# Kernel optimization log

Hardware: AMD Instinct MI355X
Metric: run time of the kernel (lower is better)

The kernel has to match this reference:

```python
import jax, jax.numpy as jnp
import numpy as np

TEMPERATURE = 0.04
LAMBDA_KOLEO = 0.1
EPS_NORM = 1e-12
EPS_KOLEO = 1e-9


def setup_inputs() -> dict:
    key = jax.random.key(0)
    k1, k2 = jax.random.split(key)
    N, D = 8192, 512
    z1 = jax.random.normal(k1, (N, D), dtype=jnp.float32)
    z2 = jax.random.normal(k2, (N, D), dtype=jnp.float32)
    return {"z1": z1, "z2": z2}


def _l2_normalize(x):
    # matches F.normalize(x, dim=1) with default eps=1e-12
    n = jnp.linalg.norm(x, axis=1, keepdims=True)
    return x / jnp.maximum(n, EPS_NORM)


def _infonce(queries, keys, temperature):
    # [N, N] similarity logits; labels are the diagonal
    logits = (queries @ keys.T) / temperature
    logp = jax.nn.log_softmax(logits, axis=1)
    return -jnp.mean(jnp.diagonal(logp))


def _koleo(emb):
    # pairwise euclidean distances via gram trick (matches torch.cdist p=2)
    sq = jnp.sum(emb * emb, axis=1)
    d2 = sq[:, None] + sq[None, :] - 2.0 * (emb @ emb.T)
    d = jnp.sqrt(jnp.maximum(d2, 0.0))
    N = emb.shape[0]
    eye = jnp.eye(N, dtype=bool)
    d = jnp.where(eye, jnp.inf, d)
    min_d = jnp.min(d, axis=1)
    return -jnp.mean(jnp.log(min_d + EPS_KOLEO))


def reference(z1, z2):
    z1 = _l2_normalize(z1)
    z2 = _l2_normalize(z2)
    loss_12 = _infonce(z1, z2, TEMPERATURE)
    loss_21 = _infonce(z2, z1, TEMPERATURE)
    loss_contrastive = (loss_12 + loss_21) / 2
    koleo_1 = _koleo(z1)
    koleo_2 = _koleo(z2)
    loss_koleo = (koleo_1 + koleo_2) / 2
    total_loss = loss_contrastive + LAMBDA_KOLEO * loss_koleo
    return total_loss
```

## Files before the change

### kernel.cpp

```cpp
#include <hip/hip_runtime.h>
#include <hip/hip_bf16.h>
#include <hip/hip_fp8.h>
#include <math.h>

#define N 8192
#define D 512
#define BM 128
#define BK 64
#define NSTRIP 64
#define S_BLOCKS (NSTRIP * NSTRIP)
#define TRI (NSTRIP * (NSTRIP + 1) / 2)
#define G_BLOCKS (2 * TRI)
#define SG_BLOCKS (S_BLOCKS + G_BLOCKS)

typedef float f32x4 __attribute__((ext_vector_type(4)));
typedef long l2 __attribute__((ext_vector_type(2)));

__device__ inline void gload_lds16(const void* g, void* l) {
  __builtin_amdgcn_global_load_lds(
      (const __attribute__((address_space(1))) void*)g,
      (__attribute__((address_space(3))) void*)l, 16, 0, 0);
}

__global__ __launch_bounds__(256) void norm_kernel(
    const float* __restrict__ z1, const float* __restrict__ z2,
    unsigned char* __restrict__ q1, unsigned char* __restrict__ q2,
    float* __restrict__ diag, float* __restrict__ out) {
  int row = blockIdx.x;
  int t = threadIdx.x;
  if (row == 0 && t == 0) out[0] = 0.0f;
  const float* a = z1 + (size_t)row * D;
  const float* b = z2 + (size_t)row * D;
  float va[2], vb[2];
  float ss1 = 0.f, ss2 = 0.f, dd = 0.f;
#pragma unroll
  for (int i = 0; i < 2; i++) {
    float x = a[t + 256 * i];
    float y = b[t + 256 * i];
    va[i] = x; vb[i] = y;
    ss1 += x * x; ss2 += y * y; dd += x * y;
  }
#pragma unroll
  for (int off = 1; off < 64; off <<= 1) {
    ss1 += __shfl_xor(ss1, off);
    ss2 += __shfl_xor(ss2, off);
    dd  += __shfl_xor(dd,  off);
  }
  __shared__ float red[3][4];
  int wv = t >> 6;
  if ((t & 63) == 0) { red[0][wv] = ss1; red[1][wv] = ss2; red[2][wv] = dd; }
  __syncthreads();
  ss1 = red[0][0] + red[0][1] + red[0][2] + red[0][3];
  ss2 = red[1][0] + red[1][1] + red[1][2] + red[1][3];
  dd  = red[2][0] + red[2][1] + red[2][2] + red[2][3];
  float i1 = 1.0f / fmaxf(sqrtf(ss1), 1e-12f);
  float i2 = 1.0f / fmaxf(sqrtf(ss2), 1e-12f);
#pragma unroll
  for (int i = 0; i < 2; i++) {
    __hip_fp8_e4m3 c1((float)(va[i] * i1));
    __hip_fp8_e4m3 c2((float)(vb[i] * i2));
    q1[(size_t)row * D + t + 256 * i] = c1.__x;
    q2[(size_t)row * D + t + 256 * i] = c2.__x;
  }
  if (t == 0) diag[row] = dd * i1 * i2;
}

__device__ __forceinline__ void mm_tile_fp8(
    const unsigned char* __restrict__ X, const unsigned char* __restrict__ Y,
    int r0, int c0, unsigned char* At, unsigned char* Bt, f32x4 (&acc)[4][4],
    int t, int lr, int quad, int rw, int cw) {
  const f32x4 vzero = {0.0f, 0.0f, 0.0f, 0.0f};
#pragma unroll
  for (int i = 0; i < 4; i++)
#pragma unroll
    for (int j = 0; j < 4; j++) acc[i][j] = vzero;

  for (int kc = 0; kc < 8; kc++) {
    int k0 = kc * BK;
    __syncthreads();
#pragma unroll
    for (int it = 0; it < 2; it++) {
      int s = it * 256 + t;
      int row = s >> 2, cs = s & 3;
      int src = cs ^ ((row >> 1) & 3);
      gload_lds16(X + (size_t)(r0 + row) * D + k0 + src * 16, &At[s * 16]);
    }
#pragma unroll
    for (int it = 0; it < 2; it++) {
      int s = it * 256 + t;
      int row = s >> 2, cs = s & 3;
      int src = cs ^ ((row >> 1) & 3);
      gload_lds16(Y + (size_t)(c0 + row) * D + k0 + src * 16, &Bt[s * 16]);
    }
    __syncthreads();

    l2 af[4], bf[4];
#pragma unroll
    for (int i = 0; i < 4; i++) {
      int row = rw * 64 + i * 16 + lr;
      int ps = quad ^ ((row >> 1) & 3);
      af[i] = *(const l2*)&At[row * 64 + ps * 16];
    }
#pragma unroll
    for (int j = 0; j < 4; j++) {
      int row = cw * 64 + j * 16 + lr;
      int ps = quad ^ ((row >> 1) & 3);
      bf[j] = *(const l2*)&Bt[row * 64 + ps * 16];
    }
#pragma unroll
    for (int i = 0; i < 4; i++)
#pragma unroll
      for (int j = 0; j < 4; j++)
        acc[i][j] = __builtin_amdgcn_mfma_f32_16x16x32_fp8_fp8(af[i].x, bf[j].x, acc[i][j], 0, 0, 0);
#pragma unroll
    for (int i = 0; i < 4; i++)
#pragma unroll
      for (int j = 0; j < 4; j++)
        acc[i][j] = __builtin_amdgcn_mfma_f32_16x16x32_fp8_fp8(af[i].y, bf[j].y, acc[i][j], 0, 0, 0);
  }
}

__global__ __launch_bounds__(256, 3) void sg_kernel(
    const unsigned char* __restrict__ q1, const unsigned char* __restrict__ q2,
    float* __restrict__ rowS, float* __restrict__ colS,
    float* __restrict__ partG) {
  __shared__ unsigned char At[BM * BK];
  __shared__ unsigned char Bt[BM * BK];
  __shared__ float redA[2][BM];
  __shared__ float redB[2][BM];

  int bx = blockIdx.x;
  int t = threadIdx.x;
  int lane = t & 63;
  int wave = t >> 6;
  int quad = lane >> 4;
  int lr = lane & 15;
  int rw = wave >> 1;
  int cw = wave & 1;
  const float scale = 1.4426950408889634f / 0.04f;

  bool smode = bx < S_BLOCKS;
  const unsigned char* X;
  const unsigned char* Y;
  int r0, c0, ga = 0, gb = 0, gg = 0;
  bool diagb = false;
  if (smode) {
    r0 = (bx >> 6) * BM;
    c0 = (bx & 63) * BM;
    X = q1; Y = q2;
  } else {
    int gx = bx - S_BLOCKS;
    gg = (gx >= TRI) ? 1 : 0;
    int tri = gx - gg * TRI;
    int a = (int)((sqrtf(8.0f * (float)tri + 1.0f) - 1.0f) * 0.5f);
    while ((a + 1) * (a + 2) / 2 <= tri) a++;
    while (a * (a + 1) / 2 > tri) a--;
    int b = tri - a * (a + 1) / 2;
    ga = a; gb = b;
    X = gg ? q2 : q1; Y = X;
    r0 = a * BM;
    c0 = b * BM;
    diagb = (a == b);
  }

  f32x4 acc[4][4];
  mm_tile_fp8(X, Y, r0, c0, At, Bt, acc, t, lr, quad, rw, cw);

  if (smode) {
    float rowacc[4][4];
    float colacc[4] = {0.0f, 0.0f, 0.0f, 0.0f};
#pragma unroll
    for (int i = 0; i < 4; i++)
#pragma unroll
      for (int r = 0; r < 4; r++) rowacc[i][r] = 0.0f;
#pragma unroll
    for (int i = 0; i < 4; i++)
#pragma unroll
      for (int j = 0; j < 4; j++)
#pragma unroll
        for (int r = 0; r < 4; r++) {
          float e = __builtin_amdgcn_exp2f(acc[i][j][r] * scale);
          rowacc[i][r] += e;
          colacc[j] += e;
        }
#pragma unroll
    for (int j = 0; j < 4; j++) {
      colacc[j] += __shfl_xor(colacc[j], 16);
      colacc[j] += __shfl_xor(colacc[j], 32);
    }
    if (lane < 16) {
#pragma unroll
      for (int j = 0; j < 4; j++) redA[rw][cw * 64 + j * 16 + lr] = colacc[j];
    }
    __syncthreads();
    if (t < BM) colS[(size_t)(r0 >> 7) * N + c0 + t] = redA[0][t] + redA[1][t];

#pragma unroll
    for (int i = 0; i < 4; i++)
#pragma unroll
      for (int r = 0; r < 4; r++) {
        float v = rowacc[i][r];
#pragma unroll
        for (int off = 1; off < 16; off <<= 1) v += __shfl_xor(v, off);
        if (lr == 0) redB[cw][rw * 64 + i * 16 + quad * 4 + r] = v;
      }
    __syncthreads();
    if (t < BM) rowS[(size_t)(c0 >> 7) * N + r0 + t] = redB[0][t] + redB[1][t];
  } else {
#pragma unroll
    for (int i = 0; i < 4; i++)
#pragma unroll
      for (int r = 0; r < 4; r++) {
        int rr = rw * 64 + i * 16 + quad * 4 + r;
        float v = -3.0e38f;
#pragma unroll
        for (int j = 0; j < 4; j++) {
          float x = acc[i][j][r];
          int cc = cw * 64 + j * 16 + lr;
          if (diagb && cc == rr) x = -3.0e38f;
          v = fmaxf(v, x);
        }
#pragma unroll
        for (int off = 1; off < 16; off <<= 1) v = fmaxf(v, __shfl_xor(v, off));
        if (lr == 0) redA[cw][rr] = v;
      }
    __syncthreads();
    if (t < BM)
      partG[((size_t)(gg * NSTRIP + gb)) * N + r0 + t] = fmaxf(redA[0][t], redA[1][t]);

    if (!diagb) {
#pragma unroll
      for (int j = 0; j < 4; j++) {
        float m = acc[0][j][0];
#pragma unroll
        for (int i = 0; i < 4; i++)
#pragma unroll
          for (int r = 0; r < 4; r++) m = fmaxf(m, acc[i][j][r]);
        m = fmaxf(m, __shfl_xor(m, 16));
        m = fmaxf(m, __shfl_xor(m, 32));
        if (lane < 16) redB[rw][cw * 64 + j * 16 + lr] = m;
      }
      __syncthreads();
      if (t < BM)
        partG[((size_t)(gg * NSTRIP + ga)) * N + c0 + t] = fmaxf(redB[0][t], redB[1][t]);
    }
  }
}

__global__ __launch_bounds__(256) void combine_kernel(
    const float* __restrict__ diag,
    const float* __restrict__ rowS, const float* __restrict__ colS,
    const float* __restrict__ partG, float* __restrict__ out) {
  const float invT = 25.0f;
  int i = blockIdx.x * 256 + threadIdx.x;

  float s = 0.0f;
  for (int q = 0; q < NSTRIP; q++) s += rowS[(size_t)q * N + i];
  float a12 = logf(s) - diag[i] * invT;

  s = 0.0f;
  for (int o = 0; o < NSTRIP; o++) s += colS[(size_t)o * N + i];
  float a21 = logf(s) - diag[i] * invT;

  float g1 = -3.0e38f, g2 = -3.0e38f;
  for (int o = 0; o < NSTRIP; o++) {
    g1 = fmaxf(g1, partG[(size_t)o * N + i]);
    g2 = fmaxf(g2, partG[(size_t)(NSTRIP + o) * N + i]);
  }
  float k1 = logf(sqrtf(fmaxf(2.0f - 2.0f * g1, 0.0f)) + 1e-9f);
  float k2 = logf(sqrtf(fmaxf(2.0f - 2.0f * g2, 0.0f)) + 1e-9f);

  float c = 0.5f * (a12 + a21) / (float)N - 0.1f * 0.5f * (k1 + k2) / (float)N;
#pragma unroll
  for (int off = 1; off < 64; off <<= 1) c += __shfl_xor(c, off);
  __shared__ float fr[4];
  int wv = threadIdx.x >> 6;
  if ((threadIdx.x & 63) == 0) fr[wv] = c;
  __syncthreads();
  if (threadIdx.x == 0)
    atomicAdd(out, fr[0] + fr[1] + fr[2] + fr[3]);
}

extern "C" void kernel_launch(void* const* d_in, const int* in_sizes, int n_in,
                              void* d_out, int out_size, void* d_ws, size_t ws_size,
                              hipStream_t stream) {
  const float* z1 = (const float*)d_in[0];
  const float* z2 = (const float*)d_in[1];
  char* w = (char*)d_ws;
  unsigned char* q1 = (unsigned char*)w; w += (size_t)N * D;
  unsigned char* q2 = (unsigned char*)w; w += (size_t)N * D;
  float* diag = (float*)w;   w += (size_t)N * sizeof(float);
  float* rowS = (float*)w;   w += (size_t)NSTRIP * N * sizeof(float);
  float* colS = (float*)w;   w += (size_t)NSTRIP * N * sizeof(float);
  float* partG = (float*)w;  w += (size_t)2 * NSTRIP * N * sizeof(float);
  float* out = (float*)d_out;

  norm_kernel<<<N, 256, 0, stream>>>(z1, z2, q1, q2, diag, out);
  sg_kernel<<<SG_BLOCKS, 256, 0, stream>>>(q1, q2, rowS, colS, partG);
  combine_kernel<<<N / 256, 256, 0, stream>>>(diag, rowS, colS, partG, out);
}
```

Before: 190.7 us.

## Switch similarity GEMMs from fp8 to int8 MFMA with per-row scales

Quantizes normalized rows to int8 using a per-row absmax scale instead of fp8 e4m3, and runs the GEMMs with the int8 16x16x64 MFMA and a 128-byte K tile. The per-row scales are stored and applied in the epilogue before the exp and max reductions. The aim is to take advantage of int8 MFMA throughput and fewer K iterations, at the cost of extra scale loads and multiplies in the epilogue and doubled LDS tiles, which may lower occupancy.

```diff
diff --git a/kernel.cpp b/kernel.cpp
--- a/kernel.cpp
+++ b/kernel.cpp
@@ -1,20 +1,18 @@
 #include <hip/hip_runtime.h>
 #include <hip/hip_bf16.h>
-#include <hip/hip_fp8.h>
 #include <math.h>
 
 #define N 8192
 #define D 512
 #define BM 128
-#define BK 64
+#define BKB 128
 #define NSTRIP 64
 #define S_BLOCKS (NSTRIP * NSTRIP)
 #define TRI (NSTRIP * (NSTRIP + 1) / 2)
 #define G_BLOCKS (2 * TRI)
 #define SG_BLOCKS (S_BLOCKS + G_BLOCKS)
 
-typedef float f32x4 __attribute__((ext_vector_type(4)));
-typedef long l2 __attribute__((ext_vector_type(2)));
+typedef int i32x4 __attribute__((ext_vector_type(4)));
 
 __device__ inline void gload_lds16(const void* g, void* l) {
   __builtin_amdgcn_global_load_lds(
@@ -25,6 +23,7 @@
 __global__ __launch_bounds__(256) void norm_kernel(
     const float* __restrict__ z1, const float* __restrict__ z2,
     unsigned char* __restrict__ q1, unsigned char* __restrict__ q2,
+    float* __restrict__ invs1, float* __restrict__ invs2,
     float* __restrict__ diag, float* __restrict__ out) {
   int row = blockIdx.x;
   int t = threadIdx.x;
@@ -55,77 +54,97 @@
   dd  = red[2][0] + red[2][1] + red[2][2] + red[2][3];
   float i1 = 1.0f / fmaxf(sqrtf(ss1), 1e-12f);
   float i2 = 1.0f / fmaxf(sqrtf(ss2), 1e-12f);
+  float m1 = 1e-30f, m2 = 1e-30f;
 #pragma unroll
   for (int i = 0; i < 2; i++) {
-    __hip_fp8_e4m3 c1((float)(va[i] * i1));
-    __hip_fp8_e4m3 c2((float)(vb[i] * i2));
-    q1[(size_t)row * D + t + 256 * i] = c1.__x;
-    q2[(size_t)row * D + t + 256 * i] = c2.__x;
-  }
-  if (t == 0) diag[row] = dd * i1 * i2;
-}
-
-__device__ __forceinline__ void mm_tile_fp8(
+    m1 = fmaxf(m1, fabsf(va[i] * i1));
+    m2 = fmaxf(m2, fabsf(vb[i] * i2));
+  }
+#pragma unroll
+  for (int off = 1; off < 64; off <<= 1) {
+    m1 = fmaxf(m1, __shfl_xor(m1, off));
+    m2 = fmaxf(m2, __shfl_xor(m2, off));
+  }
+  __syncthreads();
+  if ((t & 63) == 0) { red[0][wv] = m1; red[1][wv] = m2; }
+  __syncthreads();
+  m1 = fmaxf(fmaxf(red[0][0], red[0][1]), fmaxf(red[0][2], red[0][3]));
+  m2 = fmaxf(fmaxf(red[1][0], red[1][1]), fmaxf(red[1][2], red[1][3]));
+  float s1 = 127.0f / m1, s2 = 127.0f / m2;
+#pragma unroll
+  for (int i = 0; i < 2; i++) {
+    int qa = __float2int_rn(va[i] * i1 * s1);
+    int qb = __float2int_rn(vb[i] * i2 * s2);
+    q1[(size_t)row * D + t + 256 * i] = (unsigned char)qa;
+    q2[(size_t)row * D + t + 256 * i] = (unsigned char)qb;
+  }
+  if (t == 0) {
+    diag[row] = dd * i1 * i2;
+    invs1[row] = m1 * (1.0f / 127.0f);
+    invs2[row] = m2 * (1.0f / 127.0f);
+  }
+}
+
+__device__ __forceinline__ void mm_tile_i8(
     const unsigned char* __restrict__ X, const unsigned char* __restrict__ Y,
-    int r0, int c0, unsigned char* At, unsigned char* Bt, f32x4 (&acc)[4][4],
+    int r0, int c0, unsigned char* At, unsigned char* Bt, i32x4 (&acc)[4][4],
     int t, int lr, int quad, int rw, int cw) {
-  const f32x4 vzero = {0.0f, 0.0f, 0.0f, 0.0f};
+  const i32x4 izero = {0, 0, 0, 0};
 #pragma unroll
   for (int i = 0; i < 4; i++)
 #pragma unroll
-    for (int j = 0; j < 4; j++) acc[i][j] = vzero;
-
-  for (int kc = 0; kc < 8; kc++) {
-    int k0 = kc * BK;
-    __syncthreads();
-#pragma unroll
-    for (int it = 0; it < 2; it++) {
+    for (int j = 0; j < 4; j++) acc[i][j] = izero;
+
+  for (int kc = 0; kc < 4; kc++) {
+    int k0 = kc * BKB;
+    __syncthreads();
+#pragma unroll
+    for (int it = 0; it < 4; it++) {
       int s = it * 256 + t;
-      int row = s >> 2, cs = s & 3;
-      int src = cs ^ ((row >> 1) & 3);
+      int row = s >> 3, cs = s & 7;
+      int src = cs ^ (row & 7);
       gload_lds16(X + (size_t)(r0 + row) * D + k0 + src * 16, &At[s * 16]);
     }
 #pragma unroll
-    for (int it = 0; it < 2; it++) {
+    for (int it = 0; it < 4; it++) {
       int s = it * 256 + t;
-      int row = s >> 2, cs = s & 3;
-      int src = cs ^ ((row >> 1) & 3);
+      int row = s >> 3, cs = s & 7;
+      int src = cs ^ (row & 7);
       gload_lds16(Y + (size_t)(c0 + row) * D + k0 + src * 16, &Bt[s * 16]);
     }
     __syncthreads();
 
-    l2 af[4], bf[4];
-#pragma unroll
-    for (int i = 0; i < 4; i++) {
-      int row = rw * 64 + i * 16 + lr;
-      int ps = quad ^ ((row >> 1) & 3);
-      af[i] = *(const l2*)&At[row * 64 + ps * 16];
-    }
-#pragma unroll
-    for (int j = 0; j < 4; j++) {
-      int row = cw * 64 + j * 16 + lr;
-      int ps = quad ^ ((row >> 1) & 3);
-      bf[j] = *(const l2*)&Bt[row * 64 + ps * 16];
-    }
-#pragma unroll
-    for (int i = 0; i < 4; i++)
-#pragma unroll
-      for (int j = 0; j < 4; j++)
-        acc[i][j] = __builtin_amdgcn_mfma_f32_16x16x32_fp8_fp8(af[i].x, bf[j].x, acc[i][j], 0, 0, 0);
-#pragma unroll
-    for (int i = 0; i < 4; i++)
-#pragma unroll
-      for (int j = 0; j < 4; j++)
-        acc[i][j] = __builtin_amdgcn_mfma_f32_16x16x32_fp8_fp8(af[i].y, bf[j].y, acc[i][j], 0, 0, 0);
+#pragma unroll
+    for (int step = 0; step < 2; step++) {
+      i32x4 af[4], bf[4];
+#pragma unroll
+      for (int i = 0; i < 4; i++) {
+        int row = rw * 64 + i * 16 + lr;
+        int ps = (step * 4 + quad) ^ (row & 7);
+        af[i] = *(const i32x4*)&At[row * BKB + ps * 16];
+      }
+#pragma unroll
+      for (int j = 0; j < 4; j++) {
+        int row = cw * 64 + j * 16 + lr;
+        int ps = (step * 4 + quad) ^ (row & 7);
+        bf[j] = *(const i32x4*)&Bt[row * BKB + ps * 16];
+      }
+#pragma unroll
+      for (int i = 0; i < 4; i++)
+#pragma unroll
+        for (int j = 0; j < 4; j++)
+          acc[i][j] = __builtin_amdgcn_mfma_i32_16x16x64_i8(af[i], bf[j], acc[i][j], 0, 0, 0);
+    }
   }
 }
 
 __global__ __launch_bounds__(256, 3) void sg_kernel(
     const unsigned char* __restrict__ q1, const unsigned char* __restrict__ q2,
+    const float* __restrict__ invs1, const float* __restrict__ invs2,
     float* __restrict__ rowS, float* __restrict__ colS,
     float* __restrict__ partG) {
-  __shared__ unsigned char At[BM * BK];
-  __shared__ unsigned char Bt[BM * BK];
+  __shared__ unsigned char At[BM * BKB];
+  __shared__ unsigned char Bt[BM * BKB];
   __shared__ float redA[2][BM];
   __shared__ float redB[2][BM];
 
@@ -137,17 +156,19 @@
   int lr = lane & 15;
   int rw = wave >> 1;
   int cw = wave & 1;
-  const float scale = 1.4426950408889634f / 0.04f;
+  const float scalefac = 1.4426950408889634f / 0.04f;
 
   bool smode = bx < S_BLOCKS;
   const unsigned char* X;
   const unsigned char* Y;
+  const float* ivA;
+  const float* ivB;
   int r0, c0, ga = 0, gb = 0, gg = 0;
   bool diagb = false;
   if (smode) {
     r0 = (bx >> 6) * BM;
     c0 = (bx & 63) * BM;
-    X = q1; Y = q2;
+    X = q1; Y = q2; ivA = invs1; ivB = invs2;
   } else {
     int gx = bx - S_BLOCKS;
     gg = (gx >= TRI) ? 1 : 0;
@@ -158,13 +179,25 @@
     int b = tri - a * (a + 1) / 2;
     ga = a; gb = b;
     X = gg ? q2 : q1; Y = X;
+    ivA = gg ? invs2 : invs1; ivB = ivA;
     r0 = a * BM;
     c0 = b * BM;
     diagb = (a == b);
   }
 
-  f32x4 acc[4][4];
-  mm_tile_fp8(X, Y, r0, c0, At, Bt, acc, t, lr, quad, rw, cw);
+  i32x4 acc[4][4];
+  mm_tile_i8(X, Y, r0, c0, At, Bt, acc, t, lr, quad, rw, cw);
+
+  float ia[4][4];
+  float ib[4];
+#pragma unroll
+  for (int i = 0; i < 4; i++)
+#pragma unroll
+    for (int r = 0; r < 4; r++)
+      ia[i][r] = ivA[r0 + rw * 64 + i * 16 + quad * 4 + r];
+#pragma unroll
+  for (int j = 0; j < 4; j++)
+    ib[j] = ivB[c0 + cw * 64 + j * 16 + lr];
 
   if (smode) {
     float rowacc[4][4];
@@ -174,12 +207,14 @@
 #pragma unroll
       for (int r = 0; r < 4; r++) rowacc[i][r] = 0.0f;
 #pragma unroll
+    for (int j = 0; j < 4; j++) ib[j] *= scalefac;
+#pragma unroll
     for (int i = 0; i < 4; i++)
 #pragma unroll
       for (int j = 0; j < 4; j++)
 #pragma unroll
         for (int r = 0; r < 4; r++) {
-          float e = __builtin_amdgcn_exp2f(acc[i][j][r] * scale);
+          float e = __builtin_amdgcn_exp2f((float)acc[i][j][r] * ia[i][r] * ib[j]);
           rowacc[i][r] += e;
           colacc[j] += e;
         }
@@ -215,14 +250,14 @@
         float v = -3.0e38f;
 #pragma unroll
         for (int j = 0; j < 4; j++) {
-          float x = acc[i][j][r];
+          float x = (float)acc[i][j][r] * ib[j];
           int cc = cw * 64 + j * 16 + lr;
           if (diagb && cc == rr) x = -3.0e38f;
           v = fmaxf(v, x);
         }
 #pragma unroll
         for (int off = 1; off < 16; off <<= 1) v = fmaxf(v, __shfl_xor(v, off));
-        if (lr == 0) redA[cw][rr] = v;
+        if (lr == 0) redA[cw][rr] = v * ia[i][r];
       }
     __syncthreads();
     if (t < BM)
@@ -231,14 +266,14 @@
     if (!diagb) {
 #pragma unroll
       for (int j = 0; j < 4; j++) {
-        float m = acc[0][j][0];
+        float m = -3.0e38f;
 #pragma unroll
         for (int i = 0; i < 4; i++)
 #pragma unroll
-          for (int r = 0; r < 4; r++) m = fmaxf(m, acc[i][j][r]);
+          for (int r = 0; r < 4; r++) m = fmaxf(m, (float)acc[i][j][r] * ia[i][r]);
         m = fmaxf(m, __shfl_xor(m, 16));
         m = fmaxf(m, __shfl_xor(m, 32));
-        if (lane < 16) redB[rw][cw * 64 + j * 16 + lr] = m;
+        if (lane < 16) redB[rw][cw * 64 + j * 16 + lr] = m * ib[j];
       }
       __syncthreads();
       if (t < BM)
@@ -289,13 +324,15 @@
   char* w = (char*)d_ws;
   unsigned char* q1 = (unsigned char*)w; w += (size_t)N * D;
   unsigned char* q2 = (unsigned char*)w; w += (size_t)N * D;
+  float* invs1 = (float*)w;  w += (size_t)N * sizeof(float);
+  float* invs2 = (float*)w;  w += (size_t)N * sizeof(float);
   float* diag = (float*)w;   w += (size_t)N * sizeof(float);
   float* rowS = (float*)w;   w += (size_t)NSTRIP * N * sizeof(float);
   float* colS = (float*)w;   w += (size_t)NSTRIP * N * sizeof(float);
   float* partG = (float*)w;  w += (size_t)2 * NSTRIP * N * sizeof(float);
   float* out = (float*)d_out;
 
-  norm_kernel<<<N, 256, 0, stream>>>(z1, z2, q1, q2, diag, out);
-  sg_kernel<<<SG_BLOCKS, 256, 0, stream>>>(q1, q2, rowS, colS, partG);
+  norm_kernel<<<N, 256, 0, stream>>>(z1, z2, q1, q2, invs1, invs2, diag, out);
+  sg_kernel<<<SG_BLOCKS, 256, 0, stream>>>(q1, q2, invs1, invs2, rowS, colS, partG);
   combine_kernel<<<N / 256, 256, 0, stream>>>(diag, rowS, colS, partG, out);
 }
```

After: 202.2 us. +6.0%, slower.

## Load FP8 MFMA fragments directly from global memory with register double-buffering

Applied to the files above, without the earlier changes.

Removes the LDS staging tiles and the two barriers per K-chunk in the FP8 GEMM tile. Each lane now loads its MFMA A/B fragments straight from global memory (through the caches) and prefetches the next K-chunk into a second register buffer while the current one is multiplied. This frees LDS and removes synchronisation, which may help occupancy. The cost is more redundant global/L2 traffic, since waves sharing rows no longer share loads, and higher register pressure.

```diff
diff --git a/kernel.cpp b/kernel.cpp
--- a/kernel.cpp
+++ b/kernel.cpp
@@ -6,7 +6,6 @@
 #define N 8192
 #define D 512
 #define BM 128
-#define BK 64
 #define NSTRIP 64
 #define S_BLOCKS (NSTRIP * NSTRIP)
 #define TRI (NSTRIP * (NSTRIP + 1) / 2)
@@ -15,12 +14,6 @@
 
 typedef float f32x4 __attribute__((ext_vector_type(4)));
 typedef long l2 __attribute__((ext_vector_type(2)));
-
-__device__ inline void gload_lds16(const void* g, void* l) {
-  __builtin_amdgcn_global_load_lds(
-      (const __attribute__((address_space(1))) void*)g,
-      (__attribute__((address_space(3))) void*)l, 16, 0, 0);
-}
 
 __global__ __launch_bounds__(256) void norm_kernel(
     const float* __restrict__ z1, const float* __restrict__ z2,
@@ -65,58 +58,46 @@
   if (t == 0) diag[row] = dd * i1 * i2;
 }
 
-__device__ __forceinline__ void mm_tile_fp8(
+__device__ __forceinline__ void mm_tile_fp8_direct(
     const unsigned char* __restrict__ X, const unsigned char* __restrict__ Y,
-    int r0, int c0, unsigned char* At, unsigned char* Bt, f32x4 (&acc)[4][4],
-    int t, int lr, int quad, int rw, int cw) {
+    int r0, int c0, f32x4 (&acc)[4][4], int lr, int quad, int rw, int cw) {
   const f32x4 vzero = {0.0f, 0.0f, 0.0f, 0.0f};
 #pragma unroll
   for (int i = 0; i < 4; i++)
 #pragma unroll
     for (int j = 0; j < 4; j++) acc[i][j] = vzero;
 
+  const unsigned char* ap = X + (size_t)(r0 + rw * 64 + lr) * D + quad * 16;
+  const unsigned char* bp = Y + (size_t)(c0 + cw * 64 + lr) * D + quad * 16;
+
+  l2 af[2][4], bf[2][4];
+#pragma unroll
+  for (int i = 0; i < 4; i++) {
+    af[0][i] = *(const l2*)(ap + (size_t)(i * 16) * D);
+    bf[0][i] = *(const l2*)(bp + (size_t)(i * 16) * D);
+  }
   for (int kc = 0; kc < 8; kc++) {
-    int k0 = kc * BK;
-    __syncthreads();
-#pragma unroll
-    for (int it = 0; it < 2; it++) {
-      int s = it * 256 + t;
-      int row = s >> 2, cs = s & 3;
-      int src = cs ^ ((row >> 1) & 3);
-      gload_lds16(X + (size_t)(r0 + row) * D + k0 + src * 16, &At[s * 16]);
-    }
-#pragma unroll
-    for (int it = 0; it < 2; it++) {
-      int s = it * 256 + t;
-      int row = s >> 2, cs = s & 3;
-      int src = cs ^ ((row >> 1) & 3);
-      gload_lds16(Y + (size_t)(c0 + row) * D + k0 + src * 16, &Bt[s * 16]);
-    }
-    __syncthreads();
-
-    l2 af[4], bf[4];
-#pragma unroll
-    for (int i = 0; i < 4; i++) {
-      int row = rw * 64 + i * 16 + lr;
-      int ps = quad ^ ((row >> 1) & 3);
-      af[i] = *(const l2*)&At[row * 64 + ps * 16];
-    }
-#pragma unroll
-    for (int j = 0; j < 4; j++) {
-      int row = cw * 64 + j * 16 + lr;
-      int ps = quad ^ ((row >> 1) & 3);
-      bf[j] = *(const l2*)&Bt[row * 64 + ps * 16];
+    int cur = kc & 1, nxt = cur ^ 1;
+    if (kc < 7) {
+      int ko = (kc + 1) * 64;
+#pragma unroll
+      for (int i = 0; i < 4; i++) {
+        af[nxt][i] = *(const l2*)(ap + (size_t)(i * 16) * D + ko);
+        bf[nxt][i] = *(const l2*)(bp + (size_t)(i * 16) * D + ko);
+      }
     }
 #pragma unroll
     for (int i = 0; i < 4; i++)
 #pragma unroll
       for (int j = 0; j < 4; j++)
-        acc[i][j] = __builtin_amdgcn_mfma_f32_16x16x32_fp8_fp8(af[i].x, bf[j].x, acc[i][j], 0, 0, 0);
+        acc[i][j] = __builtin_amdgcn_mfma_f32_16x16x32_fp8_fp8(
+            af[cur][i].x, bf[cur][j].x, acc[i][j], 0, 0, 0);
 #pragma unroll
     for (int i = 0; i < 4; i++)
 #pragma unroll
       for (int j = 0; j < 4; j++)
-        acc[i][j] = __builtin_amdgcn_mfma_f32_16x16x32_fp8_fp8(af[i].y, bf[j].y, acc[i][j], 0, 0, 0);
+        acc[i][j] = __builtin_amdgcn_mfma_f32_16x16x32_fp8_fp8(
+            af[cur][i].y, bf[cur][j].y, acc[i][j], 0, 0, 0);
   }
 }
 
@@ -124,8 +105,6 @@
     const unsigned char* __restrict__ q1, const unsigned char* __restrict__ q2,
     float* __restrict__ rowS, float* __restrict__ colS,
     float* __restrict__ partG) {
-  __shared__ unsigned char At[BM * BK];
-  __shared__ unsigned char Bt[BM * BK];
   __shared__ float redA[2][BM];
   __shared__ float redB[2][BM];
 
@@ -164,7 +143,7 @@
   }
 
   f32x4 acc[4][4];
-  mm_tile_fp8(X, Y, r0, c0, At, Bt, acc, t, lr, quad, rw, cw);
+  mm_tile_fp8_direct(X, Y, r0, c0, acc, lr, quad, rw, cw);
 
   if (smode) {
     float rowacc[4][4];
```

Result: slower. 344.0 us (+80.4%).
